# Kernel optimization log

Hardware: AMD Instinct MI355X
Metric: run time of the kernel (lower is better)

## Reference

```python
import jax, jax.numpy as jnp
import numpy as np

NUM_GROUPS = 32
EPS = 1e-6


def group_norm(x, gamma, beta):
    # x: (b, c, h, w) -> normalize within 32 groups over (c/g, h, w)
    b, c, h, w = x.shape
    g = NUM_GROUPS
    xg = x.reshape(b, g, c // g, h, w)
    mean = xg.mean(axis=(2, 3, 4), keepdims=True)
    var = xg.var(axis=(2, 3, 4), keepdims=True)
    xg = (xg - mean) * jax.lax.rsqrt(var + EPS)
    xn = xg.reshape(b, c, h, w)
    return xn * gamma[None, :, None, None] + beta[None, :, None, None]


def setup_inputs() -> dict:
    key = jax.random.key(0)
    ks = jax.random.split(key, 4)
    b, c, h, w = 4, 512, 64, 64
    x = jax.random.normal(ks[0], (b, c, h, w), dtype=jnp.float32)
    gamma = jnp.ones((c,), dtype=jnp.float32)
    beta = jnp.zeros((c,), dtype=jnp.float32)
    w_qkv = jax.random.normal(ks[1], (3 * c, c), dtype=jnp.float32) * (1.0 / np.sqrt(c))
    b_qkv = jnp.zeros((3 * c,), dtype=jnp.float32)
    # NOTE: original init zeroes proj weight; use small random weights so the
    # attention path contributes to output/gradients in the baseline.
    w_proj = jax.random.normal(ks[2], (c, c), dtype=jnp.float32) * 0.02
    b_proj = jnp.zeros((c,), dtype=jnp.float32)
    return {"x": x, "gamma": gamma, "beta": beta, "w_qkv": w_qkv,
            "b_qkv": b_qkv, "w_proj": w_proj, "b_proj": b_proj}


def reference(x, gamma, beta, w_qkv, b_qkv, w_proj, b_proj):
    b, c, h, w = x.shape
    scale = c ** (-0.25)
    identity = x
    xn = group_norm(x, gamma, beta)
    # 1x1 conv == channel matmul: (b,c,h,w) x (3c,c) -> (b,3c,h,w)
    qkv = jnp.einsum('bchw,oc->bohw', xn, w_qkv) + b_qkv[None, :, None, None]
    qkv = qkv.reshape(b, 3 * c, h * w)
    q, k, v = jnp.split(qkv, 3, axis=1)          # each (b, c, N)
    attn = jnp.einsum('bci,bcj->bij', q * scale, k * scale)  # (b, N, N)
    attn = jax.nn.softmax(attn, axis=-1)
    out = jnp.einsum('bij,bcj->bci', attn, v)    # (b, c, N)
    out = out.reshape(b, c, h, w)
    out = jnp.einsum('bchw,oc->bohw', out, w_proj) + b_proj[None, :, None, None]
    return out + identity
```

## Files before the change

kernel.cpp:

```cpp
#include <hip/hip_runtime.h>
#include <hip/hip_fp8.h>
#include <stdint.h>

typedef unsigned short u16;
typedef unsigned char u8;
typedef __bf16 bf16x8 __attribute__((ext_vector_type(8)));
typedef float f32x4 __attribute__((ext_vector_type(4)));

__device__ __forceinline__ u16 f2bf(float f) {
  union { float f; unsigned u; } v; v.f = f;
  return (u16)((v.u + 0x7FFFu + ((v.u >> 16) & 1u)) >> 16);
}
__device__ __forceinline__ u8 f2f8(float f) {
  __hip_fp8_e4m3 h(f);
  return (u8)h.__x;
}

__device__ __forceinline__ void gld_lds16(const void* g, void* l) {
  uint32_t lo = (uint32_t)(uintptr_t)l;
  lo = __builtin_amdgcn_readfirstlane(lo);
  auto* lp = (__attribute__((address_space(3))) uint32_t*)(uintptr_t)lo;
  auto* gp = (const __attribute__((address_space(1))) uint32_t*)(uintptr_t)g;
  __builtin_amdgcn_global_load_lds(gp, lp, 16, 0, 0);
}

__global__ __launch_bounds__(256) void cvt_weights(
    const float* __restrict__ wq, const float* __restrict__ wp,
    u16* __restrict__ oq, u16* __restrict__ op) {
  int i = blockIdx.x * 256 + threadIdx.x;
  if (i < 1536 * 512) oq[i] = f2bf(wq[i]);
  if (i < 512 * 512)  op[i] = f2bf(wp[i]);
}

__global__ __launch_bounds__(256) void gn_stats(const float* __restrict__ x,
                                                float* __restrict__ stats) {
  int bg = blockIdx.x;
  const float* p = x + (size_t)bg * 65536;
  float s = 0.f, sq = 0.f;
  for (int i = threadIdx.x * 4; i < 65536; i += 1024) {
    float4 v = *(const float4*)(p + i);
    s += v.x + v.y + v.z + v.w;
    sq += v.x * v.x + v.y * v.y + v.z * v.z + v.w * v.w;
  }
  int lane = threadIdx.x & 63, w = threadIdx.x >> 6;
  for (int off = 32; off; off >>= 1) {
    s += __shfl_down(s, off);
    sq += __shfl_down(sq, off);
  }
  __shared__ float ls[4], lq[4];
  if (lane == 0) { ls[w] = s; lq[w] = sq; }
  __syncthreads();
  if (threadIdx.x == 0) {
    float S = ls[0] + ls[1] + ls[2] + ls[3];
    float Q = lq[0] + lq[1] + lq[2] + lq[3];
    float mean = S * (1.f / 65536.f);
    float var = Q * (1.f / 65536.f) - mean * mean;
    stats[bg * 2] = mean;
    stats[bg * 2 + 1] = rsqrtf(var + 1e-6f);
  }
}

__global__ __launch_bounds__(256) void gn_norm_t(const float* __restrict__ x,
    const float* __restrict__ stats, const float* __restrict__ gamma,
    const float* __restrict__ beta, u16* __restrict__ xnT) {
  __shared__ u16 tile[64][72];
  int b = blockIdx.z;
  int c0 = blockIdx.y * 64, n0 = blockIdx.x * 64;
  int t = threadIdx.x;
  int cl = t >> 2, ng = (t & 3) * 16;
  int c = c0 + cl;
  float mean = stats[(b * 32 + (c >> 4)) * 2];
  float rstd = stats[(b * 32 + (c >> 4)) * 2 + 1];
  float a = gamma[c] * rstd;
  float b2 = beta[c] - mean * a;
  const float* src = x + ((size_t)b * 512 + c) * 4096 + n0 + ng;
  u16 e[16];
  #pragma unroll
  for (int q = 0; q < 4; ++q) {
    float4 v = *(const float4*)(src + q * 4);
    e[q * 4 + 0] = f2bf(v.x * a + b2);
    e[q * 4 + 1] = f2bf(v.y * a + b2);
    e[q * 4 + 2] = f2bf(v.z * a + b2);
    e[q * 4 + 3] = f2bf(v.w * a + b2);
  }
  #pragma unroll
  for (int j = 0; j < 16; ++j) tile[ng + j][cl] = e[j];
  __syncthreads();
  int nl = t >> 2, cg = (t & 3) * 16;
  uint4 w0 = *(const uint4*)&tile[nl][cg];
  uint4 w1 = *(const uint4*)&tile[nl][cg + 8];
  u16* dst = xnT + ((size_t)b * 4096 + n0 + nl) * 512 + c0 + cg;
  *(uint4*)dst = w0;
  *(uint4*)(dst + 8) = w1;
}

template<int EPI>
__global__ __launch_bounds__(256) void gemm_nt(
    const u16* __restrict__ A, const u16* __restrict__ B,
    int lda, int ldb, int K,
    const float* __restrict__ bias, const float* __restrict__ resid,
    float scale, float* __restrict__ outF, void* __restrict__ outBv, int ldo,
    size_t azs, size_t bzs, size_t ozs) {
  __shared__ __align__(16) u16 smem[16384];
  const size_t z = blockIdx.z;
  A += z * azs; B += z * bzs;
  const int t = threadIdx.x;
  const int wave = t >> 6, lane = t & 63;
  const int wm = wave >> 1, wn = wave & 1;
  const int quad = lane >> 4, li = lane & 15;
  const int m0 = blockIdx.y * 128, n0 = blockIdx.x * 128;

  const int srow = lane >> 2;
  const int scol = (lane & 3) * 8;
  const u16* gA[2];
  const u16* gB[2];
  int ldsOff[2];
  #pragma unroll
  for (int r = 0; r < 2; ++r) {
    int rb = wave + 4 * r;
    gA[r] = A + (size_t)(m0 + rb * 16 + srow) * lda + scol;
    gB[r] = B + (size_t)(n0 + rb * 16 + srow) * ldb + scol;
    ldsOff[r] = rb * 512;
  }

  f32x4 zero = {0.f, 0.f, 0.f, 0.f};
  f32x4 acc[4][4];
  #pragma unroll
  for (int i = 0; i < 4; ++i)
    #pragma unroll
    for (int j = 0; j < 4; ++j) acc[i][j] = zero;

  #pragma unroll
  for (int r = 0; r < 2; ++r) {
    gld_lds16(gA[r], &smem[ldsOff[r]]);
    gld_lds16(gB[r], &smem[8192 + ldsOff[r]]);
  }
  __syncthreads();

  for (int kt = 0; kt < K; kt += 32) {
    const int s = (kt >> 5) & 1;
    if (kt + 32 < K) {
      const int ns = s ^ 1;
      #pragma unroll
      for (int r = 0; r < 2; ++r) {
        gld_lds16(gA[r] + kt + 32, &smem[ns * 4096 + ldsOff[r]]);
        gld_lds16(gB[r] + kt + 32, &smem[8192 + ns * 4096 + ldsOff[r]]);
      }
    }
    bf16x8 af[4], bf[4];
    #pragma unroll
    for (int i = 0; i < 4; ++i) {
      af[i] = *(const bf16x8*)&smem[s * 4096 +
               (wm * 64 + i * 16 + li) * 32 + quad * 8];
      bf[i] = *(const bf16x8*)&smem[8192 + s * 4096 +
               (wn * 64 + i * 16 + li) * 32 + quad * 8];
    }
    #pragma unroll
    for (int i = 0; i < 4; ++i)
      #pragma unroll
      for (int j = 0; j < 4; ++j)
        acc[i][j] = __builtin_amdgcn_mfma_f32_16x16x32_bf16(
            af[i], bf[j], acc[i][j], 0, 0, 0);
    __syncthreads();
  }

  if (EPI == 3) {
    outF += z * ozs; resid += z * ozs;
    #pragma unroll
    for (int i = 0; i < 4; ++i)
      #pragma unroll
      for (int j = 0; j < 4; ++j) {
        int mB = m0 + wm * 64 + i * 16 + quad * 4;
        int n = n0 + wn * 64 + j * 16 + li;
        #pragma unroll
        for (int r = 0; r < 4; ++r) {
          int m = mB + r;
          float v = acc[i][j][r] + bias[m] + resid[(size_t)m * ldo + n];
          outF[(size_t)m * ldo + n] = v;
        }
      }
    return;
  }

  u8* out8 = (u8*)outBv + z * ozs;
  u8* bnc = (u8*)smem;
  #pragma unroll
  for (int i = 0; i < 4; ++i) {
    int lm = wm * 64 + i * 16 + quad * 4;
    #pragma unroll
    for (int j = 0; j < 4; ++j) {
      int ln = wn * 64 + j * 16 + li;
      #pragma unroll
      for (int r = 0; r < 4; ++r) {
        float v = acc[i][j][r];
        u8 o;
        if (EPI == 4) o = f2f8((v + bias[n0 + ln]) * scale);
        else          o = f2f8(v + bias[m0 + lm + r]);
        bnc[(lm + r) * 144 + ln] = o;
      }
    }
  }
  __syncthreads();
  {
    int row = t >> 1, half = t & 1;
    const u8* src = &bnc[row * 144 + half * 64];
    u8* dst = out8 + (size_t)(m0 + row) * ldo + n0 + half * 64;
    #pragma unroll
    for (int cc = 0; cc < 4; ++cc)
      *(uint4*)(dst + cc * 16) = *(const uint4*)(src + cc * 16);
  }
}

template<int EPI, int SWZ>
__global__ __launch_bounds__(256) void gemm_nt8(
    const u8* __restrict__ A, const u8* __restrict__ B,
    int lda, int ldb, int K,
    const float* __restrict__ rsum, float* __restrict__ outF,
    void* __restrict__ outBv, int ldo,
    size_t azs, size_t bzs, size_t ozs) {
  __shared__ __align__(16) u8 smem[(EPI == 6) ? 34816 : 18432];
  const size_t z = blockIdx.z;
  A += z * azs; B += z * bzs;
  int bx = blockIdx.x, by = blockIdx.y;
  if (SWZ) {
    int lin = by * 32 + bx;
    int tt = lin >> 8, w = lin & 255;
    by = (tt >> 1) * 16 + (w >> 4);
    bx = (tt & 1) * 16 + (w & 15);
  }
  const int t = threadIdx.x;
  const int wave = t >> 6, lane = t & 63;
  const int wm = wave >> 1, wn = wave & 1;
  const int quad = lane >> 4, li = lane & 15;
  const int m0 = by * 128, n0 = bx * 128;

  const int srow = lane >> 1;
  const int scol = (lane & 1) * 16;
  const u8* gA = A + (size_t)(m0 + wave * 32 + srow) * lda + scol;
  const u8* gB = B + (size_t)(n0 + wave * 32 + srow) * ldb + scol;
  const int ldsOff = wave * 1024;

  f32x4 zero = {0.f, 0.f, 0.f, 0.f};
  f32x4 acc[4][4];
  #pragma unroll
  for (int i = 0; i < 4; ++i)
    #pragma unroll
    for (int j = 0; j < 4; ++j) acc[i][j] = zero;

  gld_lds16(gA, &smem[ldsOff]);
  gld_lds16(gB, &smem[8192 + ldsOff]);
  __syncthreads();

  for (int kt = 0; kt < K; kt += 32) {
    const int s = (kt >> 5) & 1;
    if (kt + 32 < K) {
      const int ns = s ^ 1;
      gld_lds16(gA + kt + 32, &smem[ns * 4096 + ldsOff]);
      gld_lds16(gB + kt + 32, &smem[8192 + ns * 4096 + ldsOff]);
    }
    long af[4], bf[4];
    #pragma unroll
    for (int i = 0; i < 4; ++i) {
      af[i] = *(const long*)&smem[s * 4096 +
               (wm * 64 + i * 16 + li) * 32 + quad * 8];
      bf[i] = *(const long*)&smem[8192 + s * 4096 +
               (wn * 64 + i * 16 + li) * 32 + quad * 8];
    }
    #pragma unroll
    for (int i = 0; i < 4; ++i)
      #pragma unroll
      for (int j = 0; j < 4; ++j)
        acc[i][j] = __builtin_amdgcn_mfma_f32_16x16x32_fp8_fp8(
            af[i], bf[j], acc[i][j], 0, 0, 0);
    __syncthreads();
  }

  {
    const float* rsF = rsum + z * 4096;
    u16* outp = (u16*)outBv + z * ozs;
    u16* b16 = (u16*)smem;
    #pragma unroll
    for (int i = 0; i < 4; ++i) {
      int lm = wm * 64 + i * 16 + quad * 4;
      float rinv[4];
      #pragma unroll
      for (int r = 0; r < 4; ++r)
        rinv[r] = __builtin_amdgcn_rcpf(rsF[m0 + lm + r]);
      #pragma unroll
      for (int j = 0; j < 4; ++j) {
        int ln = wn * 64 + j * 16 + li;
        #pragma unroll
        for (int r = 0; r < 4; ++r)
          b16[(lm + r) * 136 + ln] = f2bf(acc[i][j][r] * rinv[r]);
      }
    }
    __syncthreads();
    int row = t >> 1, half = t & 1;
    const u16* src = &b16[row * 136 + half * 64];
    u16* dst = outp + (size_t)(m0 + row) * ldo + n0 + half * 64;
    #pragma unroll
    for (int cc = 0; cc < 8; ++cc)
      *(uint4*)(dst + cc * 8) = *(const uint4*)(src + cc * 8);
  }
}

__global__ __launch_bounds__(512, 2) void qk8p(
    const u8* __restrict__ A, const u8* __restrict__ B,
    float* __restrict__ rowsum, u8* __restrict__ outE) {
  __shared__ __align__(16) u8 smem[98304];

  int gblk = (blockIdx.z * 16 + blockIdx.y) * 16 + blockIdx.x;
  int work = (gblk & 7) * 128 + (gblk >> 3);
  int z  = work >> 8;
  int wr = work & 255;
  int by = wr >> 4, bx = wr & 15;
  const int m0 = by * 256, n0 = bx * 256;
  A += (size_t)z * 4096 * 1024;
  B += (size_t)z * 4096 * 1024;
  float* rsF = rowsum + (size_t)z * 4096;
  u8* outp = outE + (size_t)z * 4096 * 4096;

  const int t = threadIdx.x;
  const int lane = t & 63, w = t >> 6;
  const int wm = w >> 2, wn = w & 3;
  const int quad = lane >> 4, li = lane & 15;

  const u8* gA[2];
  const u8* gB[2];
  uint32_t lA[2], lB[2];
  #pragma unroll
  for (int g = 0; g < 2; ++g) {
    int row = t >> 1, c = t & 1;
    gA[g] = A + (size_t)(m0 + row) * 1024 + g * 32 + c * 16;
    gB[g] = B + (size_t)(n0 + row) * 1024 + g * 32 + c * 16;
    lA[g] = g * 8192 + w * 1024;
    lB[g] = 16384 + g * 8192 + w * 1024;
  }

  const int lo = li * 32 + quad * 8;
  const uint32_t aB0 = (uint32_t)wm * 4096;
  const uint32_t bB0 = 16384 + (uint32_t)wn * 2048;

  f32x4 zero = {0.f, 0.f, 0.f, 0.f};
  f32x4 acc[8][4];
  #pragma unroll
  for (int i = 0; i < 8; ++i)
    #pragma unroll
    for (int j = 0; j < 4; ++j) acc[i][j] = zero;

  #pragma unroll
  for (int tt = 0; tt < 2; ++tt) {
    gld_lds16(gA[0] + tt * 64, &smem[tt * 32768 + lA[0]]);
    gld_lds16(gB[0] + tt * 64, &smem[tt * 32768 + lB[0]]);
    gld_lds16(gA[1] + tt * 64, &smem[tt * 32768 + lA[1]]);
    gld_lds16(gB[1] + tt * 64, &smem[tt * 32768 + lB[1]]);
  }
  asm volatile("s_waitcnt vmcnt(4)" ::: "memory");
  asm volatile("s_barrier" ::: "memory");

  uint32_t bo = 0, bp = 65536;
  #pragma unroll 1
  for (int tt = 0; tt < 8; ++tt) {
    const bool pf = tt < 6;
    const int kp = tt * 64 + 128;
    long a[8], b0[4], b1[4];

    #pragma unroll
    for (int i = 0; i < 4; ++i)
      #pragma unroll
      for (int k = 0; k < 2; ++k)
        a[i * 2 + k] = *(const long*)&smem[bo + k * 8192 + aB0 + i * 512 + lo];
    #pragma unroll
    for (int j = 0; j < 2; ++j)
      #pragma unroll
      for (int k = 0; k < 2; ++k)
        b0[j * 2 + k] = *(const long*)&smem[bo + k * 8192 + bB0 + j * 512 + lo];
    if (pf) gld_lds16(gA[0] + kp, &smem[bp + lA[0]]);
    asm volatile("s_barrier" ::: "memory");
    __builtin_amdgcn_s_setprio(1);
    #pragma unroll
    for (int i = 0; i < 4; ++i)
      #pragma unroll
      for (int j = 0; j < 2; ++j) {
        acc[i][j] = __builtin_amdgcn_mfma_f32_16x16x32_fp8_fp8(
            a[i * 2 + 0], b0[j * 2 + 0], acc[i][j], 0, 0, 0);
        acc[i][j] = __builtin_amdgcn_mfma_f32_16x16x32_fp8_fp8(
            a[i * 2 + 1], b0[j * 2 + 1], acc[i][j], 0, 0, 0);
      }
    __builtin_amdgcn_s_setprio(0);
    asm volatile("s_barrier" ::: "memory");

    #pragma unroll
    for (int j = 0; j < 2; ++j)
      #pragma unroll
      for (int k = 0; k < 2; ++k)
        b1[j * 2 + k] =
            *(const long*)&smem[bo + k * 8192 + bB0 + 1024 + j * 512 + lo];
    if (pf) gld_lds16(gB[0] + kp, &smem[bp + lB[0]]);
    asm volatile("s_barrier" ::: "memory");
    __builtin_amdgcn_s_setprio(1);
    #pragma unroll
    for (int i = 0; i < 4; ++i)
      #pragma unroll
      for (int j = 0; j < 2; ++j) {
        acc[i][2 + j] = __builtin_amdgcn_mfma_f32_16x16x32_fp8_fp8(
            a[i * 2 + 0], b1[j * 2 + 0], acc[i][2 + j], 0, 0, 0);
        acc[i][2 + j] = __builtin_amdgcn_mfma_f32_16x16x32_fp8_fp8(
            a[i * 2 + 1], b1[j * 2 + 1], acc[i][2 + j], 0, 0, 0);
      }
    __builtin_amdgcn_s_setprio(0);
    asm volatile("s_barrier" ::: "memory");

    #pragma unroll
    for (int i = 0; i < 4; ++i)
      #pragma unroll
      for (int k = 0; k < 2; ++k)
        a[i * 2 + k] =
            *(const long*)&smem[bo + k * 8192 + aB0 + 2048 + i * 512 + lo];
    if (pf) gld_lds16(gA[1] + kp, &smem[bp + lA[1]]);
    asm volatile("s_barrier" ::: "memory");
    __builtin_amdgcn_s_setprio(1);
    #pragma unroll
    for (int i = 0; i < 4; ++i)
      #pragma unroll
      for (int j = 0; j < 2; ++j) {
        acc[4 + i][2 + j] = __builtin_amdgcn_mfma_f32_16x16x32_fp8_fp8(
            a[i * 2 + 0], b1[j * 2 + 0], acc[4 + i][2 + j], 0, 0, 0);
        acc[4 + i][2 + j] = __builtin_amdgcn_mfma_f32_16x16x32_fp8_fp8(
            a[i * 2 + 1], b1[j * 2 + 1], acc[4 + i][2 + j], 0, 0, 0);
      }
    __builtin_amdgcn_s_setprio(0);
    asm volatile("s_barrier" ::: "memory");

    if (pf) {
      gld_lds16(gB[1] + kp, &smem[bp + lB[1]]);
      asm volatile("s_waitcnt vmcnt(4)" ::: "memory");
    } else {
      asm volatile("s_waitcnt vmcnt(0)" ::: "memory");
    }
    asm volatile("s_barrier" ::: "memory");
    __builtin_amdgcn_s_setprio(1);
    #pragma unroll
    for (int i = 0; i < 4; ++i)
      #pragma unroll
      for (int j = 0; j < 2; ++j) {
        acc[4 + i][j] = __builtin_amdgcn_mfma_f32_16x16x32_fp8_fp8(
            a[i * 2 + 0], b0[j * 2 + 0], acc[4 + i][j], 0, 0, 0);
        acc[4 + i][j] = __builtin_amdgcn_mfma_f32_16x16x32_fp8_fp8(
            a[i * 2 + 1], b0[j * 2 + 1], acc[4 + i][j], 0, 0, 0);
      }
    __builtin_amdgcn_s_setprio(0);
    asm volatile("s_barrier" ::: "memory");

    bo += 32768; if (bo == 98304) bo = 0;
    bp += 32768; if (bp == 98304) bp = 0;
  }

  u8* bnc = smem;
  #pragma unroll
  for (int I = 0; I < 8; ++I) {
    int lm = wm * 128 + I * 16 + quad * 4;
    float rs[4] = {0.f, 0.f, 0.f, 0.f};
    #pragma unroll
    for (int j = 0; j < 4; ++j) {
      int ln = wn * 64 + j * 16 + li;
      #pragma unroll
      for (int r = 0; r < 4; ++r) {
        float e = fminf(__expf(acc[I][j][r]), 448.f);
        bnc[(lm + r) * 272 + ln] = f2f8(e);
        rs[r] += e;
      }
    }
    #pragma unroll
    for (int r = 0; r < 4; ++r) {
      rs[r] += __shfl_xor(rs[r], 1);
      rs[r] += __shfl_xor(rs[r], 2);
      rs[r] += __shfl_xor(rs[r], 4);
      rs[r] += __shfl_xor(rs[r], 8);
    }
    if (li == 0) {
      #pragma unroll
      for (int r = 0; r < 4; ++r) atomicAdd(&rsF[m0 + lm + r], rs[r]);
    }
  }
  __syncthreads();
  {
    int row = t >> 1, half = t & 1;
    const u8* src = &bnc[row * 272 + half * 128];
    u8* dst = outp + (size_t)(m0 + row) * 4096 + n0 + half * 128;
    #pragma unroll
    for (int cc = 0; cc < 8; ++cc)
      *(uint4*)(dst + cc * 16) = *(const uint4*)(src + cc * 16);
  }
}

extern "C" void kernel_launch(void* const* d_in, const int* in_sizes, int n_in,
                              void* d_out, int out_size, void* d_ws, size_t ws_size,
                              hipStream_t stream) {
  (void)in_sizes; (void)n_in; (void)out_size; (void)ws_size;
  const float* x      = (const float*)d_in[0];
  const float* gamma  = (const float*)d_in[1];
  const float* beta   = (const float*)d_in[2];
  const float* w_qkv  = (const float*)d_in[3];
  const float* b_qkv  = (const float*)d_in[4];
  const float* w_proj = (const float*)d_in[5];
  const float* b_proj = (const float*)d_in[6];
  float* out = (float*)d_out;

  const int C = 512, N = 4096;
  const size_t NC = (size_t)N * C;
  const float scale = 0.21022410381342863f;

  char* ws = (char*)d_ws;
  size_t off = 0;
  auto alloc = [&](size_t bytes) -> char* {
    char* p = ws + off; off += (bytes + 255) & ~(size_t)255; return p;
  };
  u16*   wq_bf  = (u16*)alloc((size_t)1536 * 512 * 2);
  u16*   wp_bf  = (u16*)alloc((size_t)512 * 512 * 2);
  float* stats  = (float*)alloc(128 * 2 * 4);
  float* rowsum = (float*)alloc((size_t)4 * N * 4);
  u16*   xnT    = (u16*)alloc((size_t)4 * NC * 2);
  u8*    qkT    = (u8*)alloc((size_t)4 * N * 1024);
  u8*    vbf    = (u8*)alloc((size_t)4 * 512 * 4096);
  u16*   ao     = (u16*)alloc((size_t)4 * NC * 2);
  u8*    E      = (u8*)alloc((size_t)4 * N * N);

  cvt_weights<<<3072, 256, 0, stream>>>(w_qkv, w_proj, wq_bf, wp_bf);
  gn_stats<<<128, 256, 0, stream>>>(x, stats);
  gn_norm_t<<<dim3(64, 8, 4), 256, 0, stream>>>(x, stats, gamma, beta, xnT);
  hipMemsetAsync(rowsum, 0, (size_t)4 * N * 4, stream);

  gemm_nt<4><<<dim3(8, 32, 4), 256, 0, stream>>>(
      xnT, wq_bf, 512, 512, 512, b_qkv, nullptr, scale,
      nullptr, qkT, 1024, NC, 0, (size_t)N * 1024);
  gemm_nt<5><<<dim3(32, 4, 4), 256, 0, stream>>>(
      wq_bf + (size_t)1024 * 512, xnT, 512, 512, 512, b_qkv + 1024, nullptr,
      0.f, nullptr, vbf, 4096, 0, NC, (size_t)512 * 4096);
  qk8p<<<dim3(16, 16, 4), 512, 0, stream>>>(qkT, qkT + 512, rowsum, E);
  gemm_nt8<6, 0><<<dim3(4, 32, 4), 256, 0, stream>>>(
      E, vbf, 4096, 4096, 4096, rowsum, nullptr,
      ao, 512, (size_t)N * N, (size_t)512 * 4096, NC);
  gemm_nt<3><<<dim3(32, 4, 4), 256, 0, stream>>>(
      wp_bf, ao, 512, 512, 512, b_proj, x, 0.f,
      out, nullptr, 4096, 0, NC, NC);
}
```

Before: 444.6 us.

## Swizzle LDS tile layout and triple-buffer the fp8 NT GEMM pipeline

Measured after the change: 428.3 us. 3.7% less time.

```diff
diff --git a/kernel.cpp b/kernel.cpp
--- a/kernel.cpp
+++ b/kernel.cpp
@@ -218,7 +218,7 @@
     const float* __restrict__ rsum, float* __restrict__ outF,
     void* __restrict__ outBv, int ldo,
     size_t azs, size_t bzs, size_t ozs) {
-  __shared__ __align__(16) u8 smem[(EPI == 6) ? 34816 : 18432];
+  __shared__ __align__(16) u8 smem[(EPI == 6) ? 34816 : 24576];
   const size_t z = blockIdx.z;
   A += z * azs; B += z * bzs;
   int bx = blockIdx.x, by = blockIdx.y;
@@ -234,11 +234,22 @@
   const int quad = lane >> 4, li = lane & 15;
   const int m0 = by * 128, n0 = bx * 128;
 
-  const int srow = lane >> 1;
-  const int scol = (lane & 1) * 16;
-  const u8* gA = A + (size_t)(m0 + wave * 32 + srow) * lda + scol;
-  const u8* gB = B + (size_t)(n0 + wave * 32 + srow) * ldb + scol;
+  const int us = lane ^ ((lane >> 3) & 7);
+  const int srow = (us >> 1) & 31;
+  const int shalf = us & 1;
+  const u8* gA = A + (size_t)(m0 + wave * 32 + srow) * lda + shalf * 16;
+  const u8* gB = B + (size_t)(n0 + wave * 32 + srow) * ldb + shalf * 16;
   const int ldsOff = wave * 1024;
+
+  const int h = quad >> 1, qlo = (quad & 1) * 8;
+  int aoff[4], boff[4];
+  #pragma unroll
+  for (int i = 0; i < 4; ++i) {
+    int r5 = (i & 1) * 16 + li;
+    int p = (2 * r5 + h) ^ ((r5 >> 2) & 7);
+    aoff[i] = (wm * 2 + (i >> 1)) * 1024 + p * 16 + qlo;
+    boff[i] = (wn * 2 + (i >> 1)) * 1024 + p * 16 + qlo;
+  }
 
   f32x4 zero = {0.f, 0.f, 0.f, 0.f};
   f32x4 acc[4][4];
@@ -248,23 +259,25 @@
     for (int j = 0; j < 4; ++j) acc[i][j] = zero;
 
   gld_lds16(gA, &smem[ldsOff]);
-  gld_lds16(gB, &smem[8192 + ldsOff]);
-  __syncthreads();
-
+  gld_lds16(gB, &smem[12288 + ldsOff]);
+  gld_lds16(gA + 32, &smem[4096 + ldsOff]);
+  gld_lds16(gB + 32, &smem[12288 + 4096 + ldsOff]);
+  asm volatile("s_waitcnt vmcnt(2)" ::: "memory");
+  asm volatile("s_barrier" ::: "memory");
+
+  int s = 0;
   for (int kt = 0; kt < K; kt += 32) {
-    const int s = (kt >> 5) & 1;
-    if (kt + 32 < K) {
-      const int ns = s ^ 1;
-      gld_lds16(gA + kt + 32, &smem[ns * 4096 + ldsOff]);
-      gld_lds16(gB + kt + 32, &smem[8192 + ns * 4096 + ldsOff]);
-    }
+    if (kt + 64 < K) {
+      const int ns = (s == 0) ? 2 : s - 1;
+      gld_lds16(gA + kt + 64, &smem[ns * 4096 + ldsOff]);
+      gld_lds16(gB + kt + 64, &smem[12288 + ns * 4096 + ldsOff]);
+    }
+    const int sb = s * 4096;
     long af[4], bf[4];
     #pragma unroll
     for (int i = 0; i < 4; ++i) {
-      af[i] = *(const long*)&smem[s * 4096 +
-               (wm * 64 + i * 16 + li) * 32 + quad * 8];
-      bf[i] = *(const long*)&smem[8192 + s * 4096 +
-               (wn * 64 + i * 16 + li) * 32 + quad * 8];
+      af[i] = *(const long*)&smem[sb + aoff[i]];
+      bf[i] = *(const long*)&smem[12288 + sb + boff[i]];
     }
     #pragma unroll
     for (int i = 0; i < 4; ++i)
@@ -272,8 +285,14 @@
       for (int j = 0; j < 4; ++j)
         acc[i][j] = __builtin_amdgcn_mfma_f32_16x16x32_fp8_fp8(
             af[i], bf[j], acc[i][j], 0, 0, 0);
-    __syncthreads();
-  }
+    if (kt + 32 < K) {
+      if (kt + 64 < K) asm volatile("s_waitcnt vmcnt(2)" ::: "memory");
+      else             asm volatile("s_waitcnt vmcnt(0)" ::: "memory");
+      asm volatile("s_barrier" ::: "memory");
+    }
+    s = (s == 2) ? 0 : s + 1;
+  }
+  __syncthreads();
 
   {
     const float* rsF = rsum + z * 4096;
@@ -325,19 +344,34 @@
   const int wm = w >> 2, wn = w & 3;
   const int quad = lane >> 4, li = lane & 15;
 
+  const int us = lane ^ ((lane >> 3) & 7);
+  const int srow = (us >> 1) & 31;
+  const int shalf = us & 1;
   const u8* gA[2];
   const u8* gB[2];
   uint32_t lA[2], lB[2];
   #pragma unroll
   for (int g = 0; g < 2; ++g) {
-    int row = t >> 1, c = t & 1;
-    gA[g] = A + (size_t)(m0 + row) * 1024 + g * 32 + c * 16;
-    gB[g] = B + (size_t)(n0 + row) * 1024 + g * 32 + c * 16;
+    gA[g] = A + (size_t)(m0 + w * 32 + srow) * 1024 + g * 32 + shalf * 16;
+    gB[g] = B + (size_t)(n0 + w * 32 + srow) * 1024 + g * 32 + shalf * 16;
     lA[g] = g * 8192 + w * 1024;
     lB[g] = 16384 + g * 8192 + w * 1024;
   }
 
-  const int lo = li * 32 + quad * 8;
+  const int h = quad >> 1, qlo = (quad & 1) * 8;
+  int pa[4], pb[2];
+  #pragma unroll
+  for (int i = 0; i < 4; ++i) {
+    int r5 = (i & 1) * 16 + li;
+    int p = (2 * r5 + h) ^ ((r5 >> 2) & 7);
+    pa[i] = (i >> 1) * 1024 + p * 16 + qlo;
+  }
+  #pragma unroll
+  for (int j = 0; j < 2; ++j) {
+    int r5 = j * 16 + li;
+    int p = (2 * r5 + h) ^ ((r5 >> 2) & 7);
+    pb[j] = p * 16 + qlo;
+  }
   const uint32_t aB0 = (uint32_t)wm * 4096;
   const uint32_t bB0 = 16384 + (uint32_t)wn * 2048;
 
@@ -369,12 +403,12 @@
     for (int i = 0; i < 4; ++i)
       #pragma unroll
       for (int k = 0; k < 2; ++k)
-        a[i * 2 + k] = *(const long*)&smem[bo + k * 8192 + aB0 + i * 512 + lo];
+        a[i * 2 + k] = *(const long*)&smem[bo + k * 8192 + aB0 + pa[i]];
     #pragma unroll
     for (int j = 0; j < 2; ++j)
       #pragma unroll
       for (int k = 0; k < 2; ++k)
-        b0[j * 2 + k] = *(const long*)&smem[bo + k * 8192 + bB0 + j * 512 + lo];
+        b0[j * 2 + k] = *(const long*)&smem[bo + k * 8192 + bB0 + pb[j]];
     if (pf) gld_lds16(gA[0] + kp, &smem[bp + lA[0]]);
     asm volatile("s_barrier" ::: "memory");
     __builtin_amdgcn_s_setprio(1);
@@ -395,7 +429,7 @@
       #pragma unroll
       for (int k = 0; k < 2; ++k)
         b1[j * 2 + k] =
-            *(const long*)&smem[bo + k * 8192 + bB0 + 1024 + j * 512 + lo];
+            *(const long*)&smem[bo + k * 8192 + bB0 + 1024 + pb[j]];
     if (pf) gld_lds16(gB[0] + kp, &smem[bp + lB[0]]);
     asm volatile("s_barrier" ::: "memory");
     __builtin_amdgcn_s_setprio(1);
@@ -416,7 +450,7 @@
       #pragma unroll
       for (int k = 0; k < 2; ++k)
         a[i * 2 + k] =
-            *(const long*)&smem[bo + k * 8192 + aB0 + 2048 + i * 512 + lo];
+            *(const long*)&smem[bo + k * 8192 + aB0 + 2048 + pa[i]];
     if (pf) gld_lds16(gA[1] + kp, &smem[bp + lA[1]]);
     asm volatile("s_barrier" ::: "memory");
     __builtin_amdgcn_s_setprio(1);
```
